# Performance work log

Measured on AMD Instinct MI355X. Metric: run time of the kernel, lower is better.

## Reference

```python
import jax, jax.numpy as jnp
import numpy as np

M = 262144          # total lanes
N_GROUPS = 32768    # unique obstacle ids (static; original uses torch.unique)
H = 64              # lane_hidden_size
I = 64              # lane_info_enc_size
F = 64              # lane_future_enc_size
SOFT_ARGMAX_DEGREE = 1.0


def setup_inputs() -> dict:
    key = jax.random.key(0)
    k = jax.random.split(key, 8)
    lane_ht = jax.random.normal(k[0], (M, H), jnp.float32)
    lane_info_enc = jax.random.normal(k[1], (M, I), jnp.float32)
    lane_future_enc = jax.random.normal(k[2], (M, F), jnp.float32)
    # sorted group ids covering every group (8 lanes per obstacle)
    same_obstacle_mask = jnp.sort(jnp.arange(M, dtype=jnp.int32) % N_GROUPS).reshape(M, 1)
    # lane_scoring_mlp params: Linear(128->16) + ReLU + Linear(16->1)
    W1 = jax.random.normal(k[3], (H + I, 16), jnp.float32) * 0.05
    b1 = jnp.zeros((16,), jnp.float32)
    W2 = jax.random.normal(k[4], (16, 1), jnp.float32) * 0.05
    b2 = jnp.zeros((1,), jnp.float32)
    return {"lane_ht": lane_ht, "lane_info_enc": lane_info_enc,
            "lane_future_enc": lane_future_enc,
            "W1": W1, "b1": b1, "W2": W2, "b2": b2,
            "same_obstacle_mask": same_obstacle_mask}


def reference(lane_ht, lane_info_enc, lane_future_enc, W1, b1, W2, b2, same_obstacle_mask):
    seg = same_obstacle_mask.reshape(-1)                       # [M] int group ids
    # per-lane score via small MLP
    x = jnp.concatenate([lane_ht, lane_info_enc], axis=1)      # [M, 128]
    h = jax.nn.relu(x @ W1 + b1)                               # [M, 16]
    score = (h @ W2 + b2).reshape(-1) * SOFT_ARGMAX_DEGREE     # [M]
    # per-group (segment) softmax -- exact math of the dense MxN min/max/exp/sum emulation
    smax = jax.lax.stop_gradient(
        jax.ops.segment_max(score, seg, num_segments=N_GROUPS))  # [N]
    e = jnp.exp(score - smax[seg])                             # [M]
    denom = jax.ops.segment_sum(e, seg, num_segments=N_GROUPS)  # [N]
    prob = e / denom[seg]                                      # [M]
    # softmax-weighted per-group pooling of concatenated encodings
    total = jnp.concatenate([lane_ht, lane_info_enc, lane_future_enc], axis=1)  # [M, 192]
    return jax.ops.segment_sum(total * prob[:, None], seg, num_segments=N_GROUPS)  # [N, 192]
```

## Files before the change

### kernel.cpp

```cpp
#include <hip/hip_runtime.h>


__global__ __launch_bounds__(64) void lane_attn_kernel(
    const float* __restrict__ ht,
    const float* __restrict__ info,
    const float* __restrict__ fut,
    const float* __restrict__ W1,
    const float* __restrict__ b1,
    const float* __restrict__ W2,
    const float* __restrict__ b2,
    const int*   __restrict__ seg,
    float*       __restrict__ out)
{
    const int t    = threadIdx.x;
    const int base = blockIdx.x * 64;
    const int lane = base + t;

    const float4* htp = (const float4*)(ht   + (size_t)lane * 64);
    const float4* inp = (const float4*)(info + (size_t)lane * 64);

    float4 va[16], vb[16];
#pragma unroll
    for (int k = 0; k < 16; ++k) va[k] = htp[k];
#pragma unroll
    for (int k = 0; k < 16; ++k) vb[k] = inp[k];

    float h[16];
#pragma unroll
    for (int j = 0; j < 16; ++j) h[j] = b1[j];

#pragma unroll
    for (int k4 = 0; k4 < 16; ++k4) {
        const float4 v = va[k4];
#pragma unroll
        for (int j = 0; j < 16; ++j) {
            h[j] = fmaf(v.x, W1[(k4 * 4 + 0) * 16 + j], h[j]);
            h[j] = fmaf(v.y, W1[(k4 * 4 + 1) * 16 + j], h[j]);
            h[j] = fmaf(v.z, W1[(k4 * 4 + 2) * 16 + j], h[j]);
            h[j] = fmaf(v.w, W1[(k4 * 4 + 3) * 16 + j], h[j]);
        }
    }
#pragma unroll
    for (int k4 = 0; k4 < 16; ++k4) {
        const float4 v = vb[k4];
#pragma unroll
        for (int j = 0; j < 16; ++j) {
            h[j] = fmaf(v.x, W1[(64 + k4 * 4 + 0) * 16 + j], h[j]);
            h[j] = fmaf(v.y, W1[(64 + k4 * 4 + 1) * 16 + j], h[j]);
            h[j] = fmaf(v.z, W1[(64 + k4 * 4 + 2) * 16 + j], h[j]);
            h[j] = fmaf(v.w, W1[(64 + k4 * 4 + 3) * 16 + j], h[j]);
        }
    }

    float score = b2[0];
#pragma unroll
    for (int j = 0; j < 16; ++j)
        score = fmaf(fmaxf(h[j], 0.0f), W2[j], score);

    float m = score;
    m = fmaxf(m, __shfl_xor(m, 1));
    m = fmaxf(m, __shfl_xor(m, 2));
    m = fmaxf(m, __shfl_xor(m, 4));
    float e = __expf(score - m);
    float s = e;
    s += __shfl_xor(s, 1);
    s += __shfl_xor(s, 2);
    s += __shfl_xor(s, 4);
    const float prob = e / s;

    const int c = t;
    for (int gg = 0; gg < 8; ++gg) {
        const int r0  = base + gg * 8;
        const int gid = seg[r0];
        float a0 = 0.0f, a1 = 0.0f, a2 = 0.0f;
#pragma unroll
        for (int i = 0; i < 8; ++i) {
            const float  p = __shfl(prob, gg * 8 + i);
            const size_t r = (size_t)(r0 + i) * 64;
            a0 = fmaf(p, ht[r + c],   a0);
            a1 = fmaf(p, info[r + c], a1);
            a2 = fmaf(p, fut[r + c],  a2);
        }
        float* o = out + (size_t)gid * 192;
        o[c]       = a0;
        o[64 + c]  = a1;
        o[128 + c] = a2;
    }
}

extern "C" void kernel_launch(void* const* d_in, const int* in_sizes, int n_in,
                              void* d_out, int out_size, void* d_ws, size_t ws_size,
                              hipStream_t stream) {
    const float* ht   = (const float*)d_in[0];
    const float* info = (const float*)d_in[1];
    const float* fut  = (const float*)d_in[2];
    const float* W1   = (const float*)d_in[3];
    const float* b1   = (const float*)d_in[4];
    const float* W2   = (const float*)d_in[5];
    const float* b2   = (const float*)d_in[6];
    const int*   seg  = (const int*)d_in[7];
    float*       out  = (float*)d_out;

    const int M = in_sizes[7];
    const int blocks = M / 64;

    lane_attn_kernel<<<blocks, 64, 0, stream>>>(ht, info, fut, W1, b1, W2, b2,
                                                seg, out);
}
```

Measured before the change: 236.0 us.

## Stage lane rows through skewed LDS tile for coalesced loads and vectorize pooling

Input rows are now loaded with coalesced float4 accesses across the wavefront, then transposed through a 16 KB shared-memory tile with a rotation skew to avoid bank conflicts. Each thread still reads its own row for the MLP dot product. The old per-thread strided row loads were poorly coalesced. The pooling stage now uses float4 loads over four rows at once plus a cross-quarter shuffle reduction. This adds LDS traffic, manual waitcnt fences without a barrier (valid only because the block is a single wavefront), and extra shuffles.

```diff
diff --git a/kernel.cpp b/kernel.cpp
--- a/kernel.cpp
+++ b/kernel.cpp
@@ -1,5 +1,7 @@
 #include <hip/hip_runtime.h>
 
+
+#define LGKM_FENCE() asm volatile("s_waitcnt lgkmcnt(0)" ::: "memory")
 
 __global__ __launch_bounds__(64) void lane_attn_kernel(
     const float* __restrict__ ht,
@@ -12,43 +14,77 @@
     const int*   __restrict__ seg,
     float*       __restrict__ out)
 {
+    __shared__ float tile[64 * 64];
+
     const int t    = threadIdx.x;
     const int base = blockIdx.x * 64;
-    const int lane = base + t;
 
-    const float4* htp = (const float4*)(ht   + (size_t)lane * 64);
-    const float4* inp = (const float4*)(info + (size_t)lane * 64);
+    const float4* ht4 = (const float4*)ht;
+    const float4* in4 = (const float4*)info;
+    const float4* fu4 = (const float4*)fut;
+    const int fbase = base * 16;
 
-    float4 va[16], vb[16];
+    float4 hv[16];
 #pragma unroll
-    for (int k = 0; k < 16; ++k) va[k] = htp[k];
+    for (int it = 0; it < 16; ++it) hv[it] = ht4[fbase + it * 64 + t];
+
 #pragma unroll
-    for (int k = 0; k < 16; ++k) vb[k] = inp[k];
+    for (int it = 0; it < 16; ++it) {
+        const int f  = it * 64 + t;
+        const int r  = f >> 4;
+        const int c0 = (f & 15) << 2;
+        float* rb = &tile[r * 64];
+        rb[(c0 + 0 + r) & 63] = hv[it].x;
+        rb[(c0 + 1 + r) & 63] = hv[it].y;
+        rb[(c0 + 2 + r) & 63] = hv[it].z;
+        rb[(c0 + 3 + r) & 63] = hv[it].w;
+    }
+
+    float4 iv[16];
+#pragma unroll
+    for (int it = 0; it < 16; ++it) iv[it] = in4[fbase + it * 64 + t];
+
+    LGKM_FENCE();
 
     float h[16];
 #pragma unroll
     for (int j = 0; j < 16; ++j) h[j] = b1[j];
 
+    {
+        const int rb = t * 64;
+#pragma unroll 8
+        for (int k = 0; k < 64; ++k) {
+            const float x = tile[rb + ((k + t) & 63)];
 #pragma unroll
-    for (int k4 = 0; k4 < 16; ++k4) {
-        const float4 v = va[k4];
-#pragma unroll
-        for (int j = 0; j < 16; ++j) {
-            h[j] = fmaf(v.x, W1[(k4 * 4 + 0) * 16 + j], h[j]);
-            h[j] = fmaf(v.y, W1[(k4 * 4 + 1) * 16 + j], h[j]);
-            h[j] = fmaf(v.z, W1[(k4 * 4 + 2) * 16 + j], h[j]);
-            h[j] = fmaf(v.w, W1[(k4 * 4 + 3) * 16 + j], h[j]);
+            for (int j = 0; j < 16; ++j)
+                h[j] = fmaf(x, W1[k * 16 + j], h[j]);
         }
     }
+
+    LGKM_FENCE();
+
 #pragma unroll
-    for (int k4 = 0; k4 < 16; ++k4) {
-        const float4 v = vb[k4];
+    for (int it = 0; it < 16; ++it) {
+        const int f  = it * 64 + t;
+        const int r  = f >> 4;
+        const int c0 = (f & 15) << 2;
+        float* rb = &tile[r * 64];
+        rb[(c0 + 0 + r) & 63] = iv[it].x;
+        rb[(c0 + 1 + r) & 63] = iv[it].y;
+        rb[(c0 + 2 + r) & 63] = iv[it].z;
+        rb[(c0 + 3 + r) & 63] = iv[it].w;
+    }
+
+    LGKM_FENCE();
+
+    {
+        const int rb = t * 64;
+#pragma unroll 8
+        for (int k = 0; k < 64; ++k) {
+            const float x = tile[rb + ((k + t) & 63)];
 #pragma unroll
-        for (int j = 0; j < 16; ++j) {
-            h[j] = fmaf(v.x, W1[(64 + k4 * 4 + 0) * 16 + j], h[j]);
-            h[j] = fmaf(v.y, W1[(64 + k4 * 4 + 1) * 16 + j], h[j]);
-            h[j] = fmaf(v.z, W1[(64 + k4 * 4 + 2) * 16 + j], h[j]);
-            h[j] = fmaf(v.w, W1[(64 + k4 * 4 + 3) * 16 + j], h[j]);
+            for (int j = 0; j < 16; ++j)
+                h[j] = fmaf(x, W1[(64 + k) * 16 + j], h[j]);
         }
     }
 
@@ -68,23 +104,39 @@
     s += __shfl_xor(s, 4);
     const float prob = e / s;
 
-    const int c = t;
+    const int c4 = t & 15;
+    const int q  = t >> 4;
+
+#pragma unroll 2
     for (int gg = 0; gg < 8; ++gg) {
         const int r0  = base + gg * 8;
         const int gid = seg[r0];
-        float a0 = 0.0f, a1 = 0.0f, a2 = 0.0f;
+        float4 aH = {0.f, 0.f, 0.f, 0.f};
+        float4 aI = {0.f, 0.f, 0.f, 0.f};
+        float4 aF = {0.f, 0.f, 0.f, 0.f};
 #pragma unroll
-        for (int i = 0; i < 8; ++i) {
-            const float  p = __shfl(prob, gg * 8 + i);
-            const size_t r = (size_t)(r0 + i) * 64;
-            a0 = fmaf(p, ht[r + c],   a0);
-            a1 = fmaf(p, info[r + c], a1);
-            a2 = fmaf(p, fut[r + c],  a2);
+        for (int i2 = 0; i2 < 2; ++i2) {
+            const int row = r0 + i2 * 4 + q;
+            const float p = __shfl(prob, gg * 8 + i2 * 4 + q);
+            const float4 vh = ht4[row * 16 + c4];
+            const float4 vi = in4[row * 16 + c4];
+            const float4 vf = fu4[row * 16 + c4];
+            aH.x = fmaf(p, vh.x, aH.x); aH.y = fmaf(p, vh.y, aH.y);
+            aH.z = fmaf(p, vh.z, aH.z); aH.w = fmaf(p, vh.w, aH.w);
+            aI.x = fmaf(p, vi.x, aI.x); aI.y = fmaf(p, vi.y, aI.y);
+            aI.z = fmaf(p, vi.z, aI.z); aI.w = fmaf(p, vi.w, aI.w);
+            aF.x = fmaf(p, vf.x, aF.x); aF.y = fmaf(p, vf.y, aF.y);
+            aF.z = fmaf(p, vf.z, aF.z); aF.w = fmaf(p, vf.w, aF.w);
         }
-        float* o = out + (size_t)gid * 192;
-        o[c]       = a0;
-        o[64 + c]  = a1;
-        o[128 + c] = a2;
+#define RED(v) v += __shfl_xor(v, 16); v += __shfl_xor(v, 32)
+        RED(aH.x); RED(aH.y); RED(aH.z); RED(aH.w);
+        RED(aI.x); RED(aI.y); RED(aI.z); RED(aI.w);
+        RED(aF.x); RED(aF.y); RED(aF.z); RED(aF.w);
+#undef RED
+        float4* o = (float4*)(out + (size_t)gid * 192);
+        if (q == 0)      o[c4]      = aH;
+        else if (q == 1) o[16 + c4] = aI;
+        else if (q == 2) o[32 + c4] = aF;
     }
 }
 
```

Measured after the change: 240.8 us. 1.02x slower.
